# Optimization experiments

Measured on AMD Instinct MI355X. Metric: run time of the kernel, lower is better.

Reference implementation:

```python
import jax, jax.numpy as jnp
import numpy as np


def binarize(weight):
    # probs = tanh(weight); weight_b = +1 where probs >= 0 else -1
    probs = jnp.tanh(weight)
    return jnp.where(probs >= 0, 1.0, -1.0).astype(weight.dtype)


def setup_inputs() -> dict:
    key = jax.random.key(0)
    k1, k2 = jax.random.split(key)
    N, num_ip, num_op = 8192, 2048, 2048
    inp = jax.random.normal(k1, (N, num_ip), dtype=jnp.float32)
    # torch .uniform_() default is U[0,1)
    weight = jax.random.uniform(k2, (num_ip, num_op), dtype=jnp.float32)
    return {"input": inp, "weight": weight}


def reference(input, weight):
    weight_b = binarize(weight)  # [num_ip, num_op] in {-1, +1}
    return input @ weight_b      # [N, num_op]
```

## Files before the change

kernel.cpp:

```cpp
#include <hip/hip_runtime.h>


constexpr int NROWS = 8192;
constexpr int K     = 2048;
constexpr int NOP   = 2048;
constexpr int NSCAN = 512;
constexpr int NSUM  = 2048;
constexpr int GRPS  = K / 8;
constexpr int C4    = NOP / 4;


__global__ __launch_bounds__(256) void prep(
        const float* __restrict__ a, const float* __restrict__ w,
        unsigned char* __restrict__ dirty, float* __restrict__ rowsum,
        unsigned* __restrict__ negbits) {
    const int lane = threadIdx.x & 63;
    const int wid  = threadIdx.x >> 6;

    if (blockIdx.x < NSCAN) {
        const int b    = blockIdx.x;
        const int colb = b & 1;
        const int grp  = b >> 1;
        const int c4   = colb * 256 + threadIdx.x;
        const float4* __restrict__ w4 =
            (const float4*)(w + (size_t)(grp * 8) * NOP + c4 * 4);

        unsigned packed = 0u;
        #pragma unroll
        for (int r = 0; r < 8; ++r) {
            const float4 v = w4[r * (NOP / 4)];
            if (!(v.x >= 0.0f)) packed |= (1u << r);
            if (!(v.y >= 0.0f)) packed |= (1u << (8 + r));
            if (!(v.z >= 0.0f)) packed |= (1u << (16 + r));
            if (!(v.w >= 0.0f)) packed |= (1u << (24 + r));
        }
        negbits[(size_t)grp * C4 + c4] = packed;

        __shared__ int wd4[4];
        const int aw = __any(packed != 0u) ? 1 : 0;
        if (lane == 0) wd4[wid] = aw;
        __syncthreads();
        if (threadIdx.x == 0)
            dirty[b] = (unsigned char)(wd4[0] | wd4[1] | wd4[2] | wd4[3]);
        return;
    }

    const int n = (blockIdx.x - NSCAN) * 4 + wid;
    const float4* __restrict__ a4 = (const float4*)(a + (size_t)n * K);
    float4 v[8];
    #pragma unroll
    for (int c = 0; c < 8; ++c) v[c] = a4[c * 64 + lane];
    float s = 0.0f;
    #pragma unroll
    for (int c = 0; c < 8; ++c) s += (v[c].x + v[c].y) + (v[c].z + v[c].w);
    #pragma unroll
    for (int m = 32; m >= 1; m >>= 1) s += __shfl_xor(s, m, 64);
    if (lane == 0) rowsum[n] = s;
}

__device__ float neg_corr(const float* __restrict__ arow,
                          const unsigned* __restrict__ negbits, int o) {
    float c = 0.0f;
    const int cw = o >> 2, sh = (o & 3) * 8;
    for (int g = 0; g < GRPS; ++g) {
        unsigned m = (negbits[(size_t)g * C4 + cw] >> sh) & 0xFFu;
        while (m) { int b = __ffs(m) - 1; c += arow[g * 8 + b]; m &= m - 1; }
    }
    return c;
}

__global__ __launch_bounds__(256) void writeC(
        const float* __restrict__ a,
        const unsigned long long* __restrict__ dirty8,
        const float* __restrict__ rowsum,
        const unsigned* __restrict__ negbits,
        float* __restrict__ out) {
    const int lane = threadIdx.x & 63;
    const int wid  = threadIdx.x >> 6;
    const int n    = blockIdx.x * 4 + wid;

    const float s = rowsum[n];
    const unsigned long long dv = dirty8[lane];
    const bool dirty = __any(dv != 0ull);

    float4* __restrict__ o4 = (float4*)(out + (size_t)n * NOP);
    if (!dirty) {
        const float4 rv = make_float4(s, s, s, s);
        #pragma unroll
        for (int c = 0; c < 8; ++c) o4[c * 64 + lane] = rv;
    } else {
        const float* __restrict__ arow = a + (size_t)n * K;
        #pragma unroll 1
        for (int c = 0; c < 8; ++c) {
            const int ob = (c * 64 + lane) * 4;
            float r[4];
            #pragma unroll 1
            for (int j = 0; j < 4; ++j)
                r[j] = s - 2.0f * neg_corr(arow, negbits, ob + j);
            o4[c * 64 + lane] = make_float4(r[0], r[1], r[2], r[3]);
        }
    }
}

extern "C" void kernel_launch(void* const* d_in, const int* in_sizes, int n_in,
                              void* d_out, int out_size, void* d_ws, size_t ws_size,
                              hipStream_t stream) {
    const float* a = (const float*)d_in[0];
    const float* w = (const float*)d_in[1];
    float* out = (float*)d_out;

    unsigned char* dirty = (unsigned char*)d_ws;
    float*    rowsum  = (float*)((char*)d_ws + 1024);
    unsigned* negbits = (unsigned*)((char*)d_ws + 36864);

    prep<<<dim3(NSCAN + NSUM), dim3(256), 0, stream>>>(
        a, w, dirty, rowsum, negbits);

    writeC<<<dim3(NROWS / 4), dim3(256), 0, stream>>>(
        a, (const unsigned long long*)dirty, rowsum, negbits, out);
}
```

Before: 29.13 us.

## Write speculative all-positive output in prep kernel and shrink fixup kernel

The row-sum kernel now writes the broadcast row sum straight to the output, on the speculation that every binarized weight is +1. The second kernel becomes a small fixup that exits at once when no negative weights exist and otherwise recomputes the rows. This takes the output write out of a separate pass that had to reload row sums, and shortens the second kernel when it has nothing to do. Non-temporal stores are used for the output and the packed bits; the fixup path is slower if negatives do appear.

```diff
diff --git a/kernel.cpp b/kernel.cpp
--- a/kernel.cpp
+++ b/kernel.cpp
@@ -1,19 +1,20 @@
 #include <hip/hip_runtime.h>
 
+
+typedef float f32x4 __attribute__((ext_vector_type(4)));
 
 constexpr int NROWS = 8192;
 constexpr int K     = 2048;
 constexpr int NOP   = 2048;
 constexpr int NSCAN = 512;
-constexpr int NSUM  = 2048;
 constexpr int GRPS  = K / 8;
 constexpr int C4    = NOP / 4;
 
 
-__global__ __launch_bounds__(256) void prep(
+__global__ __launch_bounds__(256) void fused_spec(
         const float* __restrict__ a, const float* __restrict__ w,
         unsigned char* __restrict__ dirty, float* __restrict__ rowsum,
-        unsigned* __restrict__ negbits) {
+        unsigned* __restrict__ negbits, float* __restrict__ out) {
     const int lane = threadIdx.x & 63;
     const int wid  = threadIdx.x >> 6;
 
@@ -22,19 +23,19 @@
         const int colb = b & 1;
         const int grp  = b >> 1;
         const int c4   = colb * 256 + threadIdx.x;
-        const float4* __restrict__ w4 =
-            (const float4*)(w + (size_t)(grp * 8) * NOP + c4 * 4);
+        const f32x4* __restrict__ w4 =
+            (const f32x4*)(w + (size_t)(grp * 8) * NOP + c4 * 4);
 
         unsigned packed = 0u;
         #pragma unroll
         for (int r = 0; r < 8; ++r) {
-            const float4 v = w4[r * (NOP / 4)];
+            const f32x4 v = w4[(size_t)r * (NOP / 4)];
             if (!(v.x >= 0.0f)) packed |= (1u << r);
             if (!(v.y >= 0.0f)) packed |= (1u << (8 + r));
             if (!(v.z >= 0.0f)) packed |= (1u << (16 + r));
             if (!(v.w >= 0.0f)) packed |= (1u << (24 + r));
         }
-        negbits[(size_t)grp * C4 + c4] = packed;
+        __builtin_nontemporal_store(packed, &negbits[(size_t)grp * C4 + c4]);
 
         __shared__ int wd4[4];
         const int aw = __any(packed != 0u) ? 1 : 0;
@@ -46,8 +47,8 @@
     }
 
     const int n = (blockIdx.x - NSCAN) * 4 + wid;
-    const float4* __restrict__ a4 = (const float4*)(a + (size_t)n * K);
-    float4 v[8];
+    const f32x4* __restrict__ a4 = (const f32x4*)(a + (size_t)n * K);
+    f32x4 v[8];
     #pragma unroll
     for (int c = 0; c < 8; ++c) v[c] = a4[c * 64 + lane];
     float s = 0.0f;
@@ -56,6 +57,12 @@
     #pragma unroll
     for (int m = 32; m >= 1; m >>= 1) s += __shfl_xor(s, m, 64);
     if (lane == 0) rowsum[n] = s;
+
+    const f32x4 rv = {s, s, s, s};
+    f32x4* __restrict__ o4 = (f32x4*)(out + (size_t)n * NOP);
+    #pragma unroll
+    for (int c = 0; c < 8; ++c)
+        __builtin_nontemporal_store(rv, &o4[c * 64 + lane]);
 }
 
 __device__ float neg_corr(const float* __restrict__ arow,
@@ -69,36 +76,22 @@
     return c;
 }
 
-__global__ __launch_bounds__(256) void writeC(
+__global__ __launch_bounds__(256) void fixup(
         const float* __restrict__ a,
         const unsigned long long* __restrict__ dirty8,
         const float* __restrict__ rowsum,
         const unsigned* __restrict__ negbits,
         float* __restrict__ out) {
     const int lane = threadIdx.x & 63;
-    const int wid  = threadIdx.x >> 6;
-    const int n    = blockIdx.x * 4 + wid;
+    const unsigned long long dv = dirty8[lane];
+    if (!__any(dv != 0ull)) return;
 
-    const float s = rowsum[n];
-    const unsigned long long dv = dirty8[lane];
-    const bool dirty = __any(dv != 0ull);
-
-    float4* __restrict__ o4 = (float4*)(out + (size_t)n * NOP);
-    if (!dirty) {
-        const float4 rv = make_float4(s, s, s, s);
-        #pragma unroll
-        for (int c = 0; c < 8; ++c) o4[c * 64 + lane] = rv;
-    } else {
+    for (int r = 0; r < 32; ++r) {
+        const int n = blockIdx.x * 32 + r;
+        const float s = rowsum[n];
         const float* __restrict__ arow = a + (size_t)n * K;
-        #pragma unroll 1
-        for (int c = 0; c < 8; ++c) {
-            const int ob = (c * 64 + lane) * 4;
-            float r[4];
-            #pragma unroll 1
-            for (int j = 0; j < 4; ++j)
-                r[j] = s - 2.0f * neg_corr(arow, negbits, ob + j);
-            o4[c * 64 + lane] = make_float4(r[0], r[1], r[2], r[3]);
-        }
+        for (int o = threadIdx.x; o < NOP; o += 256)
+            out[(size_t)n * NOP + o] = s - 2.0f * neg_corr(arow, negbits, o);
     }
 }
 
@@ -113,9 +106,9 @@
     float*    rowsum  = (float*)((char*)d_ws + 1024);
     unsigned* negbits = (unsigned*)((char*)d_ws + 36864);
 
-    prep<<<dim3(NSCAN + NSUM), dim3(256), 0, stream>>>(
-        a, w, dirty, rowsum, negbits);
+    fused_spec<<<dim3(NSCAN + NROWS / 4), dim3(256), 0, stream>>>(
+        a, w, dirty, rowsum, negbits, out);
 
-    writeC<<<dim3(NROWS / 4), dim3(256), 0, stream>>>(
+    fixup<<<dim3(256), dim3(256), 0, stream>>>(
         a, (const unsigned long long*)dirty, rowsum, negbits, out);
 }
```

Measured after the change: 28.58 us (median of 2 runs). About the same (-1.9%).
